# Performance work log

Measured on AMD Instinct MI355X. Metric: run time of the kernel, lower is better.

## Reference

```python
import jax, jax.numpy as jnp
import numpy as np

N_NODES = 100000
N_EDGES = 1600000
DIM = 128
N_LAYERS = 3   # num_gc_layers
N_RES = 3      # residual VQ layers
N_CODE = 16    # codebook_size
N_GRAPHS = 512
BN_EPS = 1e-5
COMMIT_W = 0.25


def _l2norm(v):
    return v * jax.lax.rsqrt(jnp.sum(v * v, axis=-1, keepdims=True) + 1e-12)


def setup_inputs() -> dict:
    key = jax.random.key(0)
    ks = jax.random.split(key, 8)
    s = 0.05
    x = jax.random.normal(ks[0], (N_NODES, DIM), jnp.float32)
    edge_index = jax.random.randint(ks[1], (2, N_EDGES), 0, N_NODES)
    batch = jnp.sort(jax.random.randint(ks[2], (N_NODES,), 0, N_GRAPHS))
    W1 = jax.random.normal(ks[3], (N_LAYERS, DIM, DIM), jnp.float32) * s
    b1 = jnp.zeros((N_LAYERS, DIM), jnp.float32)
    W2 = jax.random.normal(ks[4], (N_LAYERS, DIM, DIM), jnp.float32) * s
    b2 = jnp.zeros((N_LAYERS, DIM), jnp.float32)
    gamma = jnp.ones((N_LAYERS, DIM), jnp.float32)
    beta = jnp.zeros((N_LAYERS, DIM), jnp.float32)
    codebooks = jax.random.normal(ks[5], (N_LAYERS, N_RES, N_CODE, DIM), jnp.float32)
    return dict(x=x, edge_index=edge_index, batch=batch, W1=W1, b1=b1,
                W2=W2, b2=b2, gamma=gamma, beta=beta, codebooks=codebooks)


def reference(x, edge_index, batch, W1, b1, W2, b2, gamma, beta, codebooks):
    src, dst = edge_index[0], edge_index[1]
    h = x
    xs, ids = [], []
    commit_loss = jnp.float32(0.0)
    for i in range(N_LAYERS):
        # GINConv, eps=0: MLP((1+eps)*x + sum_{j->i} x_j)
        agg = jax.ops.segment_sum(h[src], dst, num_segments=N_NODES)
        h = agg + h
        h = jax.nn.relu(h @ W1[i] + b1[i]) @ W2[i] + b2[i]  # Linear-ReLU-Linear
        h = jax.nn.relu(h)                                   # outer F.relu
        # BatchNorm1d (training-mode batch stats, biased variance)
        mean = jnp.mean(h, axis=0)
        var = jnp.var(h, axis=0)
        h = (h - mean) * jax.lax.rsqrt(var + BN_EPS) * gamma[i] + beta[i]
        xs.append(h)
        # Residual VQ with cosine-sim codebook (3 residual layers)
        r = h
        lids = []
        for l in range(N_RES):
            cbn = _l2norm(codebooks[i, l])           # [K, D] normalized codebook
            sim = _l2norm(r) @ cbn.T                  # [N, K] cosine similarity
            idx = jnp.argmax(sim, axis=-1)            # nearest code
            q = cbn[idx]                              # quantized residual
            commit_loss = commit_loss + COMMIT_W * jnp.mean(
                (jax.lax.stop_gradient(q) - r) ** 2)
            r = r - jax.lax.stop_gradient(q)
            lids.append(idx)
        ids.append(jnp.stack(lids, axis=1))           # [N, N_RES]
    xs_cat = jnp.concatenate(xs, axis=1)              # [N, DIM*N_LAYERS]
    xpool = jax.ops.segment_sum(xs_cat, batch, num_segments=N_GRAPHS)
    id_cat = jnp.concatenate(ids, axis=1)             # [N, N_RES*N_LAYERS]
    return xpool, xs_cat, commit_loss, id_cat
```

## Files before the change

kernel.cpp:

```cpp
#include <hip/hip_runtime.h>
#include <hip/hip_bf16.h>

#define N_NODES 100000
#define N_EDGES 1600000
#define DIM 128
#define NLAY 3
#define NRES 3
#define NCODE 16
#define NGRAPH 512
#define SCAN_NB ((N_NODES + 255) / 256)
#define GEMM_NB ((N_NODES + 63) / 64)

using bf16 = __hip_bfloat16;

__device__ inline void atomAddD(double* p, double v) { unsafeAtomicAdd(p, v); }

__device__ inline double ldx(const void* p, long i, int isbf) {
  if (isbf) return (double)__bfloat162float(((const bf16*)p)[i]);
  return (double)((const float*)p)[i];
}
__device__ inline void stout(void* p, long i, double v, int isbf) {
  if (isbf) ((bf16*)p)[i] = __float2bfloat16((float)v);
  else ((float*)p)[i] = (float)v;
}

__global__ void k_detect(const unsigned int* __restrict__ x, int* __restrict__ flag) {
  int tid = threadIdx.x;
  int cnt = 0;
  for (int j = tid; j < 1024; j += 256) {
    unsigned int u = x[j];
    int e = (u >> 7) & 0xFF;
    cnt += (e >= 100 && e <= 135) ? 1 : 0;
  }
  __shared__ int sh[256];
  sh[tid] = cnt; __syncthreads();
  for (int s = 128; s; s >>= 1) { if (tid < s) sh[tid] += sh[tid + s]; __syncthreads(); }
  if (tid == 0) flag[0] = (sh[0] > 512) ? 1 : 0;
}

__global__ __launch_bounds__(256) void k_convert_f(const void* __restrict__ x, float* __restrict__ hf,
                                                   long n, const int* __restrict__ flag) {
  int isbf = flag[0];
  long i = (long)blockIdx.x * 256 + threadIdx.x;
  if (i < n) hf[i] = (float)ldx(x, i, isbf);
}

__global__ __launch_bounds__(256) void k_hist(const int* __restrict__ ei, int* __restrict__ deg) {
  int e = blockIdx.x * 256 + threadIdx.x;
  if (e < N_EDGES) atomicAdd(&deg[ei[N_EDGES + e]], 1);
}

__global__ __launch_bounds__(256) void k_scan1(const int* __restrict__ deg, int* __restrict__ bsum) {
  int i = blockIdx.x * 256 + threadIdx.x;
  int v = (i < N_NODES) ? deg[i] : 0;
  for (int o = 32; o; o >>= 1) v += __shfl_xor(v, o);
  __shared__ int sh[4];
  if ((threadIdx.x & 63) == 0) sh[threadIdx.x >> 6] = v;
  __syncthreads();
  if (threadIdx.x == 0) bsum[blockIdx.x] = sh[0] + sh[1] + sh[2] + sh[3];
}

__global__ void k_scan2(int* __restrict__ bsum) {
  __shared__ int sh[512];
  int t = threadIdx.x;
  int v = (t < SCAN_NB) ? bsum[t] : 0;
  sh[t] = v; __syncthreads();
  for (int s = 1; s < 512; s <<= 1) {
    int add = (t >= s) ? sh[t - s] : 0;
    __syncthreads();
    sh[t] += add;
    __syncthreads();
  }
  if (t < SCAN_NB) bsum[t] = sh[t] - v;
}

__global__ __launch_bounds__(256) void k_scan3(const int* __restrict__ deg, const int* __restrict__ bsum,
                                               int* __restrict__ ofs, int* __restrict__ cursor) {
  int t = threadIdx.x;
  int i = blockIdx.x * 256 + t;
  int v = (i < N_NODES) ? deg[i] : 0;
  __shared__ int sh[256];
  sh[t] = v; __syncthreads();
  for (int s = 1; s < 256; s <<= 1) {
    int add = (t >= s) ? sh[t - s] : 0;
    __syncthreads();
    sh[t] += add;
    __syncthreads();
  }
  int excl = sh[t] - v + bsum[blockIdx.x];
  if (i < N_NODES) { ofs[i] = excl; cursor[i] = excl; }
  if (i == N_NODES - 1) ofs[N_NODES] = excl + v;
}

__global__ __launch_bounds__(256) void k_fill(const int* __restrict__ ei, int* __restrict__ cursor,
                                              int* __restrict__ csr) {
  int e = blockIdx.x * 256 + threadIdx.x;
  if (e < N_EDGES) {
    int d = ei[N_EDGES + e];
    int p = atomicAdd(&cursor[d], 1);
    csr[p] = ei[e];
  }
}

__global__ __launch_bounds__(256) void k_gather(const float* __restrict__ hf,
                                                const int* __restrict__ ofs,
                                                const int* __restrict__ csr,
                                                float* __restrict__ outQ) {
  int node = blockIdx.x * 4 + (threadIdx.x >> 6);
  int lane = threadIdx.x & 63;
  int beg = ofs[node], end = ofs[node + 1];
  float2 sv = *(const float2*)&hf[(long)node * DIM + lane * 2];
  double accx = (double)sv.x, accy = (double)sv.y;
  int j = beg;
  for (; j + 3 < end; j += 4) {
    int s0 = csr[j], s1 = csr[j + 1], s2 = csr[j + 2], s3 = csr[j + 3];
    float2 v0 = *(const float2*)&hf[(long)s0 * DIM + lane * 2];
    float2 v1 = *(const float2*)&hf[(long)s1 * DIM + lane * 2];
    float2 v2 = *(const float2*)&hf[(long)s2 * DIM + lane * 2];
    float2 v3 = *(const float2*)&hf[(long)s3 * DIM + lane * 2];
    accx += (double)v0.x; accy += (double)v0.y;
    accx += (double)v1.x; accy += (double)v1.y;
    accx += (double)v2.x; accy += (double)v2.y;
    accx += (double)v3.x; accy += (double)v3.y;
  }
  for (; j < end; j++) {
    int s0 = csr[j];
    float2 v0 = *(const float2*)&hf[(long)s0 * DIM + lane * 2];
    accx += (double)v0.x; accy += (double)v0.y;
  }
  *(float2*)&outQ[(long)node * DIM + lane * 2] = make_float2((float)accx, (float)accy);
}

__global__ void k_cbn(const void* __restrict__ cb, double* __restrict__ cbn, const int* __restrict__ flag) {
  int isbf = flag[0];
  int b = blockIdx.x, d = threadIdx.x;
  double v0 = ldx(cb, (long)b * DIM + d, isbf);
  double v1 = ldx(cb, (long)b * DIM + d + 64, isbf);
  double ss = v0 * v0 + v1 * v1;
  for (int o = 32; o; o >>= 1) ss += __shfl_xor(ss, o);
  double inv = 1.0 / sqrt(ss + 1e-12);
  cbn[b * DIM + d] = v0 * inv;
  cbn[b * DIM + d + 64] = v1 * inv;
}

__global__ void k_gram(const double* __restrict__ cbn, double* __restrict__ G) {
  int b = blockIdx.x, t = threadIdx.x;
  int l = b / (48 * 48); int rem = b % (48 * 48); int a = rem / 48, c = rem % 48;
  const double* ra = cbn + (long)(l * 48 + a) * DIM;
  const double* rc = cbn + (long)(l * 48 + c) * DIM;
  double s = ra[t] * rc[t] + ra[t + 64] * rc[t + 64];
  for (int o = 32; o; o >>= 1) s += __shfl_xor(s, o);
  if (t == 0) G[b] = s;
}

__global__ __launch_bounds__(256) void k_gemm_relu_f(const float* __restrict__ in,
                                                     const float* __restrict__ W,
                                                     const float* __restrict__ bias,
                                                     float* __restrict__ out) {
  __shared__ float ul[64 * DIM];
  int tid = threadIdx.x;
  long base = (long)blockIdx.x * 64;
  for (int j = tid; j < 64 * DIM / 4; j += 256) {
    long row = base + (j >> 5);
    float4 v = make_float4(0.f, 0.f, 0.f, 0.f);
    if (row < N_NODES) v = *(const float4*)&in[base * DIM + (long)j * 4];
    *(float4*)&ul[j * 4] = v;
  }
  __syncthreads();
  int cl = tid & 31;
  int rw = tid >> 5;
  int c0 = cl * 4;
  float acc[8][4] = {};
  for (int k = 0; k < DIM; k += 4) {
    float4 w0 = *(const float4*)&W[(k + 0) * DIM + c0];
    float4 w1 = *(const float4*)&W[(k + 1) * DIM + c0];
    float4 w2 = *(const float4*)&W[(k + 2) * DIM + c0];
    float4 w3 = *(const float4*)&W[(k + 3) * DIM + c0];
#pragma unroll
    for (int r = 0; r < 8; r++) {
      float4 u = *(const float4*)&ul[(rw * 8 + r) * DIM + k];
      acc[r][0] += u.x * w0.x + u.y * w1.x + u.z * w2.x + u.w * w3.x;
      acc[r][1] += u.x * w0.y + u.y * w1.y + u.z * w2.y + u.w * w3.y;
      acc[r][2] += u.x * w0.z + u.y * w1.z + u.z * w2.z + u.w * w3.z;
      acc[r][3] += u.x * w0.w + u.y * w1.w + u.z * w2.w + u.w * w3.w;
    }
  }
  float4 bv = *(const float4*)&bias[c0];
#pragma unroll
  for (int r = 0; r < 8; r++) {
    long row = base + rw * 8 + r;
    if (row < N_NODES) {
      float4 o;
      o.x = fmaxf(acc[r][0] + bv.x, 0.f);
      o.y = fmaxf(acc[r][1] + bv.y, 0.f);
      o.z = fmaxf(acc[r][2] + bv.z, 0.f);
      o.w = fmaxf(acc[r][3] + bv.w, 0.f);
      *(float4*)&out[row * DIM + c0] = o;
    }
  }
}

__global__ __launch_bounds__(256) void k_bn_stats(const float* __restrict__ h, double* __restrict__ stats) {
  int tid = threadIdx.x; int col = tid & 127; int half = tid >> 7;
  double s = 0.0, s2 = 0.0;
  for (long r = blockIdx.x * 2 + half; r < N_NODES; r += 2048) {
    double v = (double)h[r * DIM + col];
    s += v; s2 += v * v;
  }
  __shared__ double ls[256], ls2[256];
  ls[tid] = s; ls2[tid] = s2;
  __syncthreads();
  if (tid < 128) {
    atomAddD(&stats[col], ls[tid] + ls[tid + 128]);
    atomAddD(&stats[DIM + col], ls2[tid] + ls2[tid + 128]);
  }
}

__global__ void k_bn_prep(const double* __restrict__ stats, const void* __restrict__ gamma,
                          const void* __restrict__ beta, double* __restrict__ ss,
                          int l, const int* __restrict__ flag) {
  int isbf = flag[0];
  int d = threadIdx.x;
  double mean = stats[d] / (double)N_NODES;
  double var = stats[DIM + d] / (double)N_NODES - mean * mean;
  double sc = ldx(gamma, (long)l * DIM + d, isbf) / sqrt(var + 1e-5);
  ss[d] = sc;
  ss[DIM + d] = ldx(beta, (long)l * DIM + d, isbf) - mean * sc;
}

__global__ __launch_bounds__(256) void k_post(float* __restrict__ h,
                                              const double* __restrict__ ss,
                                              const int* __restrict__ batch,
                                              void* __restrict__ out,
                                              double* __restrict__ xpool,
                                              double* __restrict__ hh,
                                              int l, const int* __restrict__ flag) {
  __shared__ float hl[64 * 132];
  __shared__ double hq[64 * 4];
  __shared__ int sbat[64];
  int isbf = flag[0];
  int tid = threadIdx.x;
  long base = (long)blockIdx.x * 64;
  if (tid < 64) {
    long row = base + tid;
    sbat[tid] = (row < N_NODES) ? batch[row] : -1;
  }
  int d = tid & 127, half = tid >> 7;
  double sc = ss[d], sh = ss[DIM + d];
  const long XS_BASE = (long)NGRAPH * DIM * NLAY;
  for (int rr = half; rr < 64; rr += 2) {
    long row = base + rr;
    float vf = 0.f;
    if (row < N_NODES) {
      double v = (double)h[row * DIM + d] * sc + sh;
      vf = (float)v;
      h[row * DIM + d] = vf;
      stout(out, XS_BASE + row * (DIM * NLAY) + l * DIM + d, v, isbf);
    }
    hl[rr * 132 + d] = vf;
  }
  __syncthreads();
  {
    int row = tid >> 2, q = tid & 3;
    double s2 = 0.0;
    const float* hp = &hl[row * 132 + q * 32];
#pragma unroll
    for (int i = 0; i < 32; i++) { double v = (double)hp[i]; s2 += v * v; }
    hq[row * 4 + q] = s2;
  }
  __syncthreads();
  if (tid < 64) {
    long n = base + tid;
    if (n < N_NODES) hh[n] = hq[tid * 4] + hq[tid * 4 + 1] + hq[tid * 4 + 2] + hq[tid * 4 + 3];
  } else if (tid >= 128) {
    int dd = tid - 128;
    int g = sbat[0];
    double acc = 0.0;
    for (int r = 0; r < 64; r++) {
      int gg = sbat[r];
      if (gg < 0) break;
      if (gg != g) {
        atomAddD(&xpool[(long)g * (DIM * NLAY) + l * DIM + dd], acc);
        acc = 0.0; g = gg;
      }
      acc += (double)hl[r * 132 + dd];
    }
    atomAddD(&xpool[(long)g * (DIM * NLAY) + l * DIM + dd], acc);
  }
}

__global__ __launch_bounds__(256) void k_dotH(const float* __restrict__ hn,
                                              const double* __restrict__ cbnL,
                                              float* __restrict__ dH) {
  __shared__ double cl[48 * 134];
  int tid = threadIdx.x;
  for (int j = tid; j < 48 * DIM; j += 256) { int c = j >> 7, k = j & 127; cl[c * 134 + k] = cbnL[j]; }
  __syncthreads();
  int ct = tid & 7; int c0 = ct * 6; int rt = tid >> 3;
  long r0 = (long)blockIdx.x * 64 + rt; long r1 = r0 + 32;
  long r0c = r0 < N_NODES ? r0 : (N_NODES - 1);
  long r1c = r1 < N_NODES ? r1 : (N_NODES - 1);
  double acc0[6] = {}, acc1[6] = {};
  for (int k = 0; k < DIM; k += 4) {
    float4 h0 = *(const float4*)&hn[r0c * DIM + k];
    float4 h1 = *(const float4*)&hn[r1c * DIM + k];
#pragma unroll
    for (int j = 0; j < 6; j++) {
      double2 ca = *(const double2*)&cl[(c0 + j) * 134 + k];
      double2 cb = *(const double2*)&cl[(c0 + j) * 134 + k + 2];
      acc0[j] += (double)h0.x * ca.x + (double)h0.y * ca.y + (double)h0.z * cb.x + (double)h0.w * cb.y;
      acc1[j] += (double)h1.x * ca.x + (double)h1.y * ca.y + (double)h1.z * cb.x + (double)h1.w * cb.y;
    }
  }
  if (r0 < N_NODES) {
#pragma unroll
    for (int j = 0; j < 6; j++) dH[r0 * 48 + c0 + j] = (float)acc0[j];
  }
  if (r1 < N_NODES) {
#pragma unroll
    for (int j = 0; j < 6; j++) dH[r1 * 48 + c0 + j] = (float)acc1[j];
  }
}

__global__ __launch_bounds__(256) void k_vq(const float* __restrict__ dH, const double* __restrict__ hh,
                                            const double* __restrict__ G, void* __restrict__ out,
                                            double* __restrict__ commit, int l, const int* __restrict__ flag) {
  int isbf = flag[0];
  __shared__ double Gl[48 * 48];
  int tid = threadIdx.x;
  for (int j = tid; j < 48 * 48; j += 256) Gl[j] = G[j];
  __syncthreads();
  long n = (long)blockIdx.x * 256 + tid;
  double csum = 0.0;
  if (n < N_NODES) {
    double dh[48];
#pragma unroll
    for (int c = 0; c < 48; c++) dh[c] = (double)dH[n * 48 + c];
    int i0 = 0; double b0 = dh[0];
#pragma unroll
    for (int c = 1; c < 16; c++) { if (dh[c] > b0) { b0 = dh[c]; i0 = c; } }
    int i1 = 0; double b1 = dh[16] - Gl[i0 * 48 + 16];
#pragma unroll
    for (int c = 1; c < 16; c++) {
      double s = dh[16 + c] - Gl[i0 * 48 + 16 + c];
      if (s > b1) { b1 = s; i1 = c; }
    }
    int i2 = 0; double b2 = dh[32] - Gl[i0 * 48 + 32] - Gl[(16 + i1) * 48 + 32];
#pragma unroll
    for (int c = 1; c < 16; c++) {
      double s = dh[32 + c] - Gl[i0 * 48 + 32 + c] - Gl[(16 + i1) * 48 + 32 + c];
      if (s > b2) { b2 = s; i2 = c; }
    }
    double r1s = hh[n] - 2.0 * b0 + Gl[i0 * 48 + i0];
    double r2s = r1s - 2.0 * b1 + Gl[(16 + i1) * 48 + 16 + i1];
    double r3s = r2s - 2.0 * b2 + Gl[(32 + i2) * 48 + 32 + i2];
    csum = r1s + r2s + r3s;
    const long IDS_BASE = (long)NGRAPH * DIM * NLAY + (long)N_NODES * DIM * NLAY + 1;
    long base = IDS_BASE + n * (NLAY * NRES) + l * NRES;
    stout(out, base + 0, (double)i0, isbf);
    stout(out, base + 1, (double)i1, isbf);
    stout(out, base + 2, (double)i2, isbf);
  }
  for (int o = 32; o; o >>= 1) csum += __shfl_xor(csum, o);
  if ((tid & 63) == 0 && csum != 0.0) atomAddD(commit, csum);
}

__global__ __launch_bounds__(256) void k_out(const double* __restrict__ xpool, const double* __restrict__ commit,
                                             void* __restrict__ out, const int* __restrict__ flag) {
  int isbf = flag[0];
  long i = (long)blockIdx.x * 256 + threadIdx.x;
  const long NP = (long)NGRAPH * DIM * NLAY;
  if (i < NP) {
    stout(out, i, xpool[i], isbf);
  } else if (i == NP) {
    double c = commit[0] * (0.25 / ((double)N_NODES * (double)DIM));
    stout(out, NP + (long)N_NODES * DIM * NLAY, c, isbf);
  }
}

extern "C" void kernel_launch(void* const* d_in, const int* in_sizes, int n_in,
                              void* d_out, int out_size, void* d_ws, size_t ws_size,
                              hipStream_t stream) {
  const void* x = d_in[0];
  const int* ei = (const int*)d_in[1];
  const int* batch = (const int*)d_in[2];
  const void* W1 = d_in[3];
  const void* b1 = d_in[4];
  const void* W2 = d_in[5];
  const void* b2 = d_in[6];
  const void* gamma = d_in[7];
  const void* beta = d_in[8];
  const void* cb = d_in[9];

  double* w = (double*)d_ws;
  double* cbn = w;
  double* G = cbn + 18432;
  double* stats = G + 6912;
  double* ss = stats + 256;
  double* hh = ss + 256;
  double* xpool = hh + N_NODES;
  double* commit = xpool + (long)NGRAPH * DIM * NLAY;
  float* W1f = (float*)(commit + 2);
  float* W2f = W1f + 49152;
  float* b1f = W2f + 49152;
  float* b2f = b1f + 384;
  float* H  = b2f + 384;
  float* T1 = H + 12800000;
  float* T2 = T1 + 12800000;
  float* dH = T2 + 12800000;
  int* ibuf = (int*)(dH + 4800000);
  int* flag = ibuf;
  int* deg = ibuf + 64;
  int* ofs = deg + N_NODES;
  int* cursor = ofs + N_NODES + 1;
  int* csr = cursor + N_NODES;
  int* bsum = csr + N_EDGES;

  k_detect<<<1, 256, 0, stream>>>((const unsigned int*)x, flag);
  hipMemsetAsync(xpool, 0, ((long)NGRAPH * DIM * NLAY + 1) * sizeof(double), stream);
  hipMemsetAsync(deg, 0, N_NODES * sizeof(int), stream);
  k_convert_f<<<50000, 256, 0, stream>>>(x, H, (long)N_NODES * DIM, flag);
  k_convert_f<<<192, 256, 0, stream>>>(W1, W1f, 49152, flag);
  k_convert_f<<<192, 256, 0, stream>>>(W2, W2f, 49152, flag);
  k_convert_f<<<2, 256, 0, stream>>>(b1, b1f, 384, flag);
  k_convert_f<<<2, 256, 0, stream>>>(b2, b2f, 384, flag);
  k_cbn<<<NLAY * NRES * NCODE, 64, 0, stream>>>(cb, cbn, flag);
  k_gram<<<NLAY * 48 * 48, 64, 0, stream>>>(cbn, G);
  k_hist<<<(N_EDGES + 255) / 256, 256, 0, stream>>>(ei, deg);
  k_scan1<<<SCAN_NB, 256, 0, stream>>>(deg, bsum);
  k_scan2<<<1, 512, 0, stream>>>(bsum);
  k_scan3<<<SCAN_NB, 256, 0, stream>>>(deg, bsum, ofs, cursor);
  k_fill<<<(N_EDGES + 255) / 256, 256, 0, stream>>>(ei, cursor, csr);

  for (int l = 0; l < NLAY; l++) {
    k_gather<<<N_NODES / 4, 256, 0, stream>>>(H, ofs, csr, T1);
    k_gemm_relu_f<<<GEMM_NB, 256, 0, stream>>>(T1, W1f + l * DIM * DIM, b1f + l * DIM, T2);
    k_gemm_relu_f<<<GEMM_NB, 256, 0, stream>>>(T2, W2f + l * DIM * DIM, b2f + l * DIM, T1);
    hipMemsetAsync(stats, 0, 256 * sizeof(double), stream);
    k_bn_stats<<<1024, 256, 0, stream>>>(T1, stats);
    k_bn_prep<<<1, 128, 0, stream>>>(stats, gamma, beta, ss, l, flag);
    k_post<<<GEMM_NB, 256, 0, stream>>>(T1, ss, batch, d_out, xpool, hh, l, flag);
    k_dotH<<<1563, 256, 0, stream>>>(T1, cbn + (long)l * 48 * DIM, dH);
    k_vq<<<391, 256, 0, stream>>>(dH, hh, G + l * 48 * 48, d_out, commit, l, flag);
    float* t = H; H = T1; T1 = T2; T2 = t;
  }
  k_out<<<769, 256, 0, stream>>>(xpool, commit, d_out, flag);
}
```

Before: 1.700 ms.

## Fuse gather into first GEMM and fold BN prep and VQ into post kernel

Merges the CSR neighbour gather with the first Linear+ReLU GEMM so aggregated rows go to shared memory instead of a global T1 round trip. Folds the BN scale/shift computation, the codebook dot products and the residual VQ argmax into the post-normalisation kernel, which drops the dH and hh intermediates and three launches per layer. In exchange, each gather wave processes 16 nodes in sequence with only 16 waves per 64-row block, which may hurt latency hiding. The fused VQ now reads the codebook and Gram matrix from global memory rather than shared memory, and only 64 of 256 threads run the argmax.

```diff
diff --git a/kernel.cpp b/kernel.cpp
--- a/kernel.cpp
+++ b/kernel.cpp
@@ -102,35 +102,6 @@
   }
 }
 
-__global__ __launch_bounds__(256) void k_gather(const float* __restrict__ hf,
-                                                const int* __restrict__ ofs,
-                                                const int* __restrict__ csr,
-                                                float* __restrict__ outQ) {
-  int node = blockIdx.x * 4 + (threadIdx.x >> 6);
-  int lane = threadIdx.x & 63;
-  int beg = ofs[node], end = ofs[node + 1];
-  float2 sv = *(const float2*)&hf[(long)node * DIM + lane * 2];
-  double accx = (double)sv.x, accy = (double)sv.y;
-  int j = beg;
-  for (; j + 3 < end; j += 4) {
-    int s0 = csr[j], s1 = csr[j + 1], s2 = csr[j + 2], s3 = csr[j + 3];
-    float2 v0 = *(const float2*)&hf[(long)s0 * DIM + lane * 2];
-    float2 v1 = *(const float2*)&hf[(long)s1 * DIM + lane * 2];
-    float2 v2 = *(const float2*)&hf[(long)s2 * DIM + lane * 2];
-    float2 v3 = *(const float2*)&hf[(long)s3 * DIM + lane * 2];
-    accx += (double)v0.x; accy += (double)v0.y;
-    accx += (double)v1.x; accy += (double)v1.y;
-    accx += (double)v2.x; accy += (double)v2.y;
-    accx += (double)v3.x; accy += (double)v3.y;
-  }
-  for (; j < end; j++) {
-    int s0 = csr[j];
-    float2 v0 = *(const float2*)&hf[(long)s0 * DIM + lane * 2];
-    accx += (double)v0.x; accy += (double)v0.y;
-  }
-  *(float2*)&outQ[(long)node * DIM + lane * 2] = make_float2((float)accx, (float)accy);
-}
-
 __global__ void k_cbn(const void* __restrict__ cb, double* __restrict__ cbn, const int* __restrict__ flag) {
   int isbf = flag[0];
   int b = blockIdx.x, d = threadIdx.x;
@@ -151,6 +122,87 @@
   double s = ra[t] * rc[t] + ra[t + 64] * rc[t + 64];
   for (int o = 32; o; o >>= 1) s += __shfl_xor(s, o);
   if (t == 0) G[b] = s;
+}
+
+__global__ __launch_bounds__(256) void k_gathgemm1(const float* __restrict__ hf,
+                                                   const int* __restrict__ ofs,
+                                                   const int* __restrict__ csr,
+                                                   const float* __restrict__ W,
+                                                   const float* __restrict__ bias,
+                                                   float* __restrict__ out) {
+  __shared__ float ul[64 * DIM];
+  int tid = threadIdx.x;
+  long base = (long)blockIdx.x * 64;
+  int wave = tid >> 6, lane = tid & 63;
+  for (int i = 0; i < 16; i++) {
+    int row = wave * 16 + i;
+    long node = base + row;
+    double accx = 0.0, accy = 0.0;
+    if (node < N_NODES) {
+      int beg = ofs[node], end = ofs[node + 1];
+      float2 sv = *(const float2*)&hf[node * DIM + lane * 2];
+      accx = (double)sv.x; accy = (double)sv.y;
+      int j = beg;
+      for (; j + 7 < end; j += 8) {
+        int s0 = csr[j], s1 = csr[j + 1], s2 = csr[j + 2], s3 = csr[j + 3];
+        int s4 = csr[j + 4], s5 = csr[j + 5], s6 = csr[j + 6], s7 = csr[j + 7];
+        float2 v0 = *(const float2*)&hf[(long)s0 * DIM + lane * 2];
+        float2 v1 = *(const float2*)&hf[(long)s1 * DIM + lane * 2];
+        float2 v2 = *(const float2*)&hf[(long)s2 * DIM + lane * 2];
+        float2 v3 = *(const float2*)&hf[(long)s3 * DIM + lane * 2];
+        float2 v4 = *(const float2*)&hf[(long)s4 * DIM + lane * 2];
+        float2 v5 = *(const float2*)&hf[(long)s5 * DIM + lane * 2];
+        float2 v6 = *(const float2*)&hf[(long)s6 * DIM + lane * 2];
+        float2 v7 = *(const float2*)&hf[(long)s7 * DIM + lane * 2];
+        accx += (double)v0.x; accy += (double)v0.y;
+        accx += (double)v1.x; accy += (double)v1.y;
+        accx += (double)v2.x; accy += (double)v2.y;
+        accx += (double)v3.x; accy += (double)v3.y;
+        accx += (double)v4.x; accy += (double)v4.y;
+        accx += (double)v5.x; accy += (double)v5.y;
+        accx += (double)v6.x; accy += (double)v6.y;
+        accx += (double)v7.x; accy += (double)v7.y;
+      }
+      for (; j < end; j++) {
+        int s0 = csr[j];
+        float2 v0 = *(const float2*)&hf[(long)s0 * DIM + lane * 2];
+        accx += (double)v0.x; accy += (double)v0.y;
+      }
+    }
+    *(float2*)&ul[row * DIM + lane * 2] = make_float2((float)accx, (float)accy);
+  }
+  __syncthreads();
+  int cl = tid & 31;
+  int rw = tid >> 5;
+  int c0 = cl * 4;
+  float acc[8][4] = {};
+  for (int k = 0; k < DIM; k += 4) {
+    float4 w0 = *(const float4*)&W[(k + 0) * DIM + c0];
+    float4 w1 = *(const float4*)&W[(k + 1) * DIM + c0];
+    float4 w2 = *(const float4*)&W[(k + 2) * DIM + c0];
+    float4 w3 = *(const float4*)&W[(k + 3) * DIM + c0];
+#pragma unroll
+    for (int r = 0; r < 8; r++) {
+      float4 u = *(const float4*)&ul[(rw * 8 + r) * DIM + k];
+      acc[r][0] += u.x * w0.x + u.y * w1.x + u.z * w2.x + u.w * w3.x;
+      acc[r][1] += u.x * w0.y + u.y * w1.y + u.z * w2.y + u.w * w3.y;
+      acc[r][2] += u.x * w0.z + u.y * w1.z + u.z * w2.z + u.w * w3.z;
+      acc[r][3] += u.x * w0.w + u.y * w1.w + u.z * w2.w + u.w * w3.w;
+    }
+  }
+  float4 bv = *(const float4*)&bias[c0];
+#pragma unroll
+  for (int r = 0; r < 8; r++) {
+    long row = base + rw * 8 + r;
+    if (row < N_NODES) {
+      float4 o;
+      o.x = fmaxf(acc[r][0] + bv.x, 0.f);
+      o.y = fmaxf(acc[r][1] + bv.y, 0.f);
+      o.z = fmaxf(acc[r][2] + bv.z, 0.f);
+      o.w = fmaxf(acc[r][3] + bv.w, 0.f);
+      *(float4*)&out[row * DIM + c0] = o;
+    }
+  }
 }
 
 __global__ __launch_bounds__(256) void k_gemm_relu_f(const float* __restrict__ in,
@@ -216,37 +268,40 @@
   }
 }
 
-__global__ void k_bn_prep(const double* __restrict__ stats, const void* __restrict__ gamma,
-                          const void* __restrict__ beta, double* __restrict__ ss,
-                          int l, const int* __restrict__ flag) {
-  int isbf = flag[0];
-  int d = threadIdx.x;
-  double mean = stats[d] / (double)N_NODES;
-  double var = stats[DIM + d] / (double)N_NODES - mean * mean;
-  double sc = ldx(gamma, (long)l * DIM + d, isbf) / sqrt(var + 1e-5);
-  ss[d] = sc;
-  ss[DIM + d] = ldx(beta, (long)l * DIM + d, isbf) - mean * sc;
-}
-
-__global__ __launch_bounds__(256) void k_post(float* __restrict__ h,
-                                              const double* __restrict__ ss,
-                                              const int* __restrict__ batch,
-                                              void* __restrict__ out,
-                                              double* __restrict__ xpool,
-                                              double* __restrict__ hh,
-                                              int l, const int* __restrict__ flag) {
+__global__ __launch_bounds__(256) void k_post2(float* __restrict__ h,
+                                               const double* __restrict__ stats,
+                                               const void* __restrict__ gamma,
+                                               const void* __restrict__ beta,
+                                               const double* __restrict__ cbnL,
+                                               const double* __restrict__ Gg,
+                                               const int* __restrict__ batch,
+                                               void* __restrict__ out,
+                                               double* __restrict__ xpool,
+                                               double* __restrict__ commit,
+                                               int l, const int* __restrict__ flag) {
   __shared__ float hl[64 * 132];
+  __shared__ float dhl[64 * 49];
   __shared__ double hq[64 * 4];
+  __shared__ double ssl[256];
   __shared__ int sbat[64];
   int isbf = flag[0];
   int tid = threadIdx.x;
   long base = (long)blockIdx.x * 64;
+  if (tid < 128) {
+    int dd = tid;
+    double mean = stats[dd] / (double)N_NODES;
+    double var = stats[DIM + dd] / (double)N_NODES - mean * mean;
+    double sc = ldx(gamma, (long)l * DIM + dd, isbf) / sqrt(var + 1e-5);
+    ssl[dd] = sc;
+    ssl[DIM + dd] = ldx(beta, (long)l * DIM + dd, isbf) - mean * sc;
+  }
   if (tid < 64) {
     long row = base + tid;
     sbat[tid] = (row < N_NODES) ? batch[row] : -1;
   }
+  __syncthreads();
   int d = tid & 127, half = tid >> 7;
-  double sc = ss[d], sh = ss[DIM + d];
+  double sc = ssl[d], sh = ssl[DIM + d];
   const long XS_BASE = (long)NGRAPH * DIM * NLAY;
   for (int rr = half; rr < 64; rr += 2) {
     long row = base + rr;
@@ -261,6 +316,26 @@
   }
   __syncthreads();
   {
+    int ct = tid & 7; int c0 = ct * 6; int rt = tid >> 3;
+    double acc0[6] = {}, acc1[6] = {};
+    for (int k = 0; k < DIM; k += 4) {
+      float4 h0 = *(const float4*)&hl[rt * 132 + k];
+      float4 h1 = *(const float4*)&hl[(rt + 32) * 132 + k];
+#pragma unroll
+      for (int j = 0; j < 6; j++) {
+        double2 ca = *(const double2*)&cbnL[(long)(c0 + j) * DIM + k];
+        double2 cb = *(const double2*)&cbnL[(long)(c0 + j) * DIM + k + 2];
+        acc0[j] += (double)h0.x * ca.x + (double)h0.y * ca.y + (double)h0.z * cb.x + (double)h0.w * cb.y;
+        acc1[j] += (double)h1.x * ca.x + (double)h1.y * ca.y + (double)h1.z * cb.x + (double)h1.w * cb.y;
+      }
+    }
+#pragma unroll
+    for (int j = 0; j < 6; j++) {
+      dhl[rt * 49 + c0 + j] = (float)acc0[j];
+      dhl[(rt + 32) * 49 + c0 + j] = (float)acc1[j];
+    }
+  }
+  {
     int row = tid >> 2, q = tid & 3;
     double s2 = 0.0;
     const float* hp = &hl[row * 132 + q * 32];
@@ -271,7 +346,39 @@
   __syncthreads();
   if (tid < 64) {
     long n = base + tid;
-    if (n < N_NODES) hh[n] = hq[tid * 4] + hq[tid * 4 + 1] + hq[tid * 4 + 2] + hq[tid * 4 + 3];
+    double csum = 0.0;
+    if (n < N_NODES) {
+      double dh[48];
+#pragma unroll
+      for (int c = 0; c < 48; c++) dh[c] = (double)dhl[tid * 49 + c];
+      double hhv = hq[tid * 4] + hq[tid * 4 + 1] + hq[tid * 4 + 2] + hq[tid * 4 + 3];
+      int i0 = 0; double b0 = dh[0];
+#pragma unroll
+      for (int c = 1; c < 16; c++) { if (dh[c] > b0) { b0 = dh[c]; i0 = c; } }
+      int i1 = 0; double b1 = dh[16] - Gg[i0 * 48 + 16];
+#pragma unroll
+      for (int c = 1; c < 16; c++) {
+        double s = dh[16 + c] - Gg[i0 * 48 + 16 + c];
+        if (s > b1) { b1 = s; i1 = c; }
+      }
+      int i2 = 0; double b2 = dh[32] - Gg[i0 * 48 + 32] - Gg[(16 + i1) * 48 + 32];
+#pragma unroll
+      for (int c = 1; c < 16; c++) {
+        double s = dh[32 + c] - Gg[i0 * 48 + 32 + c] - Gg[(16 + i1) * 48 + 32 + c];
+        if (s > b2) { b2 = s; i2 = c; }
+      }
+      double r1s = hhv - 2.0 * b0 + Gg[i0 * 48 + i0];
+      double r2s = r1s - 2.0 * b1 + Gg[(16 + i1) * 48 + 16 + i1];
+      double r3s = r2s - 2.0 * b2 + Gg[(32 + i2) * 48 + 32 + i2];
+      csum = r1s + r2s + r3s;
+      const long IDS_BASE = (long)NGRAPH * DIM * NLAY + (long)N_NODES * DIM * NLAY + 1;
+      long ib = IDS_BASE + n * (NLAY * NRES) + l * NRES;
+      stout(out, ib + 0, (double)i0, isbf);
+      stout(out, ib + 1, (double)i1, isbf);
+      stout(out, ib + 2, (double)i2, isbf);
+    }
+    for (int o = 32; o; o >>= 1) csum += __shfl_xor(csum, o);
+    if (tid == 0 && csum != 0.0) atomAddD(commit, csum);
   } else if (tid >= 128) {
     int dd = tid - 128;
     int g = sbat[0];
@@ -287,82 +394,6 @@
     }
     atomAddD(&xpool[(long)g * (DIM * NLAY) + l * DIM + dd], acc);
   }
-}
-
-__global__ __launch_bounds__(256) void k_dotH(const float* __restrict__ hn,
-                                              const double* __restrict__ cbnL,
-                                              float* __restrict__ dH) {
-  __shared__ double cl[48 * 134];
-  int tid = threadIdx.x;
-  for (int j = tid; j < 48 * DIM; j += 256) { int c = j >> 7, k = j & 127; cl[c * 134 + k] = cbnL[j]; }
-  __syncthreads();
-  int ct = tid & 7; int c0 = ct * 6; int rt = tid >> 3;
-  long r0 = (long)blockIdx.x * 64 + rt; long r1 = r0 + 32;
-  long r0c = r0 < N_NODES ? r0 : (N_NODES - 1);
-  long r1c = r1 < N_NODES ? r1 : (N_NODES - 1);
-  double acc0[6] = {}, acc1[6] = {};
-  for (int k = 0; k < DIM; k += 4) {
-    float4 h0 = *(const float4*)&hn[r0c * DIM + k];
-    float4 h1 = *(const float4*)&hn[r1c * DIM + k];
-#pragma unroll
-    for (int j = 0; j < 6; j++) {
-      double2 ca = *(const double2*)&cl[(c0 + j) * 134 + k];
-      double2 cb = *(const double2*)&cl[(c0 + j) * 134 + k + 2];
-      acc0[j] += (double)h0.x * ca.x + (double)h0.y * ca.y + (double)h0.z * cb.x + (double)h0.w * cb.y;
-      acc1[j] += (double)h1.x * ca.x + (double)h1.y * ca.y + (double)h1.z * cb.x + (double)h1.w * cb.y;
-    }
-  }
-  if (r0 < N_NODES) {
-#pragma unroll
-    for (int j = 0; j < 6; j++) dH[r0 * 48 + c0 + j] = (float)acc0[j];
-  }
-  if (r1 < N_NODES) {
-#pragma unroll
-    for (int j = 0; j < 6; j++) dH[r1 * 48 + c0 + j] = (float)acc1[j];
-  }
-}
-
-__global__ __launch_bounds__(256) void k_vq(const float* __restrict__ dH, const double* __restrict__ hh,
-                                            const double* __restrict__ G, void* __restrict__ out,
-                                            double* __restrict__ commit, int l, const int* __restrict__ flag) {
-  int isbf = flag[0];
-  __shared__ double Gl[48 * 48];
-  int tid = threadIdx.x;
-  for (int j = tid; j < 48 * 48; j += 256) Gl[j] = G[j];
-  __syncthreads();
-  long n = (long)blockIdx.x * 256 + tid;
-  double csum = 0.0;
-  if (n < N_NODES) {
-    double dh[48];
-#pragma unroll
-    for (int c = 0; c < 48; c++) dh[c] = (double)dH[n * 48 + c];
-    int i0 = 0; double b0 = dh[0];
-#pragma unroll
-    for (int c = 1; c < 16; c++) { if (dh[c] > b0) { b0 = dh[c]; i0 = c; } }
-    int i1 = 0; double b1 = dh[16] - Gl[i0 * 48 + 16];
-#pragma unroll
-    for (int c = 1; c < 16; c++) {
-      double s = dh[16 + c] - Gl[i0 * 48 + 16 + c];
-      if (s > b1) { b1 = s; i1 = c; }
-    }
-    int i2 = 0; double b2 = dh[32] - Gl[i0 * 48 + 32] - Gl[(16 + i1) * 48 + 32];
-#pragma unroll
-    for (int c = 1; c < 16; c++) {
-      double s = dh[32 + c] - Gl[i0 * 48 + 32 + c] - Gl[(16 + i1) * 48 + 32 + c];
-      if (s > b2) { b2 = s; i2 = c; }
-    }
-    double r1s = hh[n] - 2.0 * b0 + Gl[i0 * 48 + i0];
-    double r2s = r1s - 2.0 * b1 + Gl[(16 + i1) * 48 + 16 + i1];
-    double r3s = r2s - 2.0 * b2 + Gl[(32 + i2) * 48 + 32 + i2];
-    csum = r1s + r2s + r3s;
-    const long IDS_BASE = (long)NGRAPH * DIM * NLAY + (long)N_NODES * DIM * NLAY + 1;
-    long base = IDS_BASE + n * (NLAY * NRES) + l * NRES;
-    stout(out, base + 0, (double)i0, isbf);
-    stout(out, base + 1, (double)i1, isbf);
-    stout(out, base + 2, (double)i2, isbf);
-  }
-  for (int o = 32; o; o >>= 1) csum += __shfl_xor(csum, o);
-  if ((tid & 63) == 0 && csum != 0.0) atomAddD(commit, csum);
 }
 
 __global__ __launch_bounds__(256) void k_out(const double* __restrict__ xpool, const double* __restrict__ commit,
@@ -396,9 +427,7 @@
   double* cbn = w;
   double* G = cbn + 18432;
   double* stats = G + 6912;
-  double* ss = stats + 256;
-  double* hh = ss + 256;
-  double* xpool = hh + N_NODES;
+  double* xpool = stats + 256;
   double* commit = xpool + (long)NGRAPH * DIM * NLAY;
   float* W1f = (float*)(commit + 2);
   float* W2f = W1f + 49152;
@@ -407,8 +436,7 @@
   float* H  = b2f + 384;
   float* T1 = H + 12800000;
   float* T2 = T1 + 12800000;
-  float* dH = T2 + 12800000;
-  int* ibuf = (int*)(dH + 4800000);
+  int* ibuf = (int*)(T2 + 12800000);
   int* flag = ibuf;
   int* deg = ibuf + 64;
   int* ofs = deg + N_NODES;
@@ -433,16 +461,14 @@
   k_fill<<<(N_EDGES + 255) / 256, 256, 0, stream>>>(ei, cursor, csr);
 
   for (int l = 0; l < NLAY; l++) {
-    k_gather<<<N_NODES / 4, 256, 0, stream>>>(H, ofs, csr, T1);
-    k_gemm_relu_f<<<GEMM_NB, 256, 0, stream>>>(T1, W1f + l * DIM * DIM, b1f + l * DIM, T2);
+    k_gathgemm1<<<GEMM_NB, 256, 0, stream>>>(H, ofs, csr, W1f + l * DIM * DIM, b1f + l * DIM, T2);
     k_gemm_relu_f<<<GEMM_NB, 256, 0, stream>>>(T2, W2f + l * DIM * DIM, b2f + l * DIM, T1);
     hipMemsetAsync(stats, 0, 256 * sizeof(double), stream);
     k_bn_stats<<<1024, 256, 0, stream>>>(T1, stats);
-    k_bn_prep<<<1, 128, 0, stream>>>(stats, gamma, beta, ss, l, flag);
-    k_post<<<GEMM_NB, 256, 0, stream>>>(T1, ss, batch, d_out, xpool, hh, l, flag);
-    k_dotH<<<1563, 256, 0, stream>>>(T1, cbn + (long)l * 48 * DIM, dH);
-    k_vq<<<391, 256, 0, stream>>>(dH, hh, G + l * 48 * 48, d_out, commit, l, flag);
-    float* t = H; H = T1; T1 = T2; T2 = t;
+    k_post2<<<GEMM_NB, 256, 0, stream>>>(T1, stats, gamma, beta,
+                                         cbn + (long)l * 48 * DIM, G + (long)l * 48 * 48,
+                                         batch, d_out, xpool, commit, l, flag);
+    float* t = H; H = T1; T1 = t;
   }
   k_out<<<769, 256, 0, stream>>>(xpool, commit, d_out, flag);
 }
```

Result: slower. 2.302 ms (+35.4%).
